# Kernel optimization log

Hardware: AMD Instinct MI355X
Metric: run time of the kernel (lower is better)

The kernel has to match this reference:

```python
import jax, jax.numpy as jnp
import numpy as np

N_NODES = 50000
N_EDGES = 400000
HID = 128
DIM_OUT = 1


def setup_inputs() -> dict:
    key = jax.random.key(0)
    ks = jax.random.split(key, 8)
    x = jax.random.normal(ks[0], (N_NODES, HID), dtype=jnp.float32)
    edge_attr = jax.random.normal(ks[1], (N_EDGES, HID), dtype=jnp.float32)
    edge_index = jax.random.randint(ks[2], (2, N_EDGES), 0, N_NODES, dtype=jnp.int64)
    # MLP params (Linear stores weight as [out,in] in torch; we use [in,out] and matmul)
    s1 = 1.0 / np.sqrt(3 * HID)
    s2 = 1.0 / np.sqrt(50)
    s3 = 1.0 / np.sqrt(25)
    W1 = jax.random.normal(ks[3], (3 * HID, 50), dtype=jnp.float32) * s1
    b1 = jnp.zeros((50,), dtype=jnp.float32)
    W2 = jax.random.normal(ks[4], (50, 25), dtype=jnp.float32) * s2
    b2 = jnp.zeros((25,), dtype=jnp.float32)
    W3 = jax.random.normal(ks[5], (25, DIM_OUT), dtype=jnp.float32) * s3
    b3 = jnp.zeros((DIM_OUT,), dtype=jnp.float32)
    return {"x": x, "edge_attr": edge_attr, "edge_index": edge_index,
            "W1": W1, "b1": b1, "W2": W2, "b2": b2, "W3": W3, "b3": b3}


def reference(x, edge_attr, edge_index, W1, b1, W2, b2, W3, b3):
    # gather endpoint features: x[edge_index.T] -> [E, 2, H] -> [E, 2H], relu
    h = jnp.take(x, edge_index.T, axis=0).reshape(-1, 2 * HID)  # [E, 2H]
    h = jax.nn.relu(h)
    h = jnp.concatenate([h, edge_attr], axis=1)  # [E, 3H]
    # 3-layer MLP (dropout = identity in eval mode)
    h = jax.nn.relu(h @ W1 + b1)
    h = jax.nn.relu(h @ W2 + b2)
    return h @ W3 + b3
```

## Files before the change

### kernel.cpp

```cpp
#include <hip/hip_runtime.h>

#define HID 128
#define PROW 104

__global__ void detect_idx_kernel(const unsigned int* __restrict__ p, int* __restrict__ flag) {
  __shared__ int s;
  if (threadIdx.x == 0) s = 0;
  __syncthreads();
  if (p[2 * threadIdx.x + 1] != 0u) atomicOr(&s, 1);
  __syncthreads();
  if (threadIdx.x == 0) *flag = s;
}

__global__ __launch_bounds__(256, 4)
void node_pre_kernel(const float* __restrict__ x, const float* __restrict__ W1,
                     float* __restrict__ P, int n_nodes) {
  __shared__ __align__(16) float a_s[32][132];
  __shared__ __align__(16) float w_s[32][64];
  const int t = threadIdx.x;
  const int half = blockIdx.y;
  const int n0 = blockIdx.x * 128;
  const int jt = t & 15, rt = t >> 4;
  float acc[8][4];
#pragma unroll
  for (int i = 0; i < 8; ++i)
#pragma unroll
    for (int q = 0; q < 4; ++q) acc[i][q] = 0.f;

  for (int kc = 0; kc < 4; ++kc) {
#pragma unroll
    for (int i = 0; i < 4; ++i) {
      int f = t + 256 * i;
      int e = f >> 3;
      int k4 = (f & 7) << 2;
      int n = n0 + e;
      float4 v = make_float4(0.f, 0.f, 0.f, 0.f);
      if (n < n_nodes) v = *(const float4*)&x[(long)n * HID + kc * 32 + k4];
      a_s[k4 + 0][e] = fmaxf(v.x, 0.f);
      a_s[k4 + 1][e] = fmaxf(v.y, 0.f);
      a_s[k4 + 2][e] = fmaxf(v.z, 0.f);
      a_s[k4 + 3][e] = fmaxf(v.w, 0.f);
    }
#pragma unroll
    for (int i = 0; i < 8; ++i) {
      int f = t + 256 * i;
      int k = f >> 6, j = f & 63;
      float w = 0.f;
      if (j < 50) w = W1[(half * 128 + kc * 32 + k) * 50 + j];
      w_s[k][j] = w;
    }
    __syncthreads();
#pragma unroll 8
    for (int kk = 0; kk < 32; ++kk) {
      float4 w4 = *(const float4*)&w_s[kk][jt * 4];
      float4 a0 = *(const float4*)&a_s[kk][rt * 8];
      float4 a1 = *(const float4*)&a_s[kk][rt * 8 + 4];
      float av[8] = {a0.x, a0.y, a0.z, a0.w, a1.x, a1.y, a1.z, a1.w};
      float wv[4] = {w4.x, w4.y, w4.z, w4.w};
#pragma unroll
      for (int ri = 0; ri < 8; ++ri)
#pragma unroll
        for (int q = 0; q < 4; ++q) acc[ri][q] = fmaf(av[ri], wv[q], acc[ri][q]);
    }
    __syncthreads();
  }
  int jb = jt * 4;
  if (jb < 50) {
#pragma unroll
    for (int ri = 0; ri < 8; ++ri) {
      int n = n0 + rt * 8 + ri;
      if (n < n_nodes) {
#pragma unroll
        for (int q = 0; q < 4; ++q) {
          int j = jb + q;
          if (j < 50) P[(long)n * PROW + half * 52 + j] = acc[ri][q];
        }
      }
    }
  }
}

__global__ __launch_bounds__(256, 4)
void edge_kernel(const float* __restrict__ ea, const void* __restrict__ eidx,
                 const float* __restrict__ W1, const float* __restrict__ b1,
                 const float* __restrict__ W2, const float* __restrict__ b2,
                 const float* __restrict__ W3, const float* __restrict__ b3,
                 const float* __restrict__ P, const int* __restrict__ flag,
                 float* __restrict__ out, int n_edges) {
  __shared__ __align__(16) union SU {
    struct { float a[32][132]; float w[32][64]; } s1;
    float h1[128][53];
  } u;
  __shared__ float w2_s[50][25];
  __shared__ float w3_s[25];
  __shared__ float b1_s[64];
  __shared__ float b2_s[25];
  __shared__ float p_s[2][128];
  __shared__ int src_s[128], dst_s[128];

  const int t = threadIdx.x;
  const int e0 = blockIdx.x * 128;

  for (int f = t; f < 1250; f += 256) ((float*)w2_s)[f] = W2[f];
  if (t < 25) { w3_s[t] = W3[t]; b2_s[t] = b2[t]; }
  if (t < 64) b1_s[t] = (t < 50) ? b1[t] : 0.f;
  const int use32 = *flag;
  if (t < 128) {
    int e = e0 + t;
    int v = 0;
    if (e < n_edges) v = use32 ? ((const int*)eidx)[e] : (int)((const long long*)eidx)[e];
    src_s[t] = v;
  } else {
    int e = e0 + (t - 128);
    int v = 0;
    if (e < n_edges)
      v = use32 ? ((const int*)eidx)[(long)n_edges + e] : (int)((const long long*)eidx)[(long)n_edges + e];
    dst_s[t - 128] = v;
  }

  const int jt = t & 15, rt = t >> 4;
  float acc[8][4];
#pragma unroll
  for (int i = 0; i < 8; ++i)
#pragma unroll
    for (int q = 0; q < 4; ++q) acc[i][q] = 0.f;

  for (int kc = 0; kc < 4; ++kc) {
#pragma unroll
    for (int i = 0; i < 4; ++i) {
      int f = t + 256 * i;
      int e = f >> 3;
      int k4 = (f & 7) << 2;
      int ee = e0 + e;
      float4 v = make_float4(0.f, 0.f, 0.f, 0.f);
      if (ee < n_edges) v = *(const float4*)&ea[(long)ee * HID + kc * 32 + k4];
      u.s1.a[k4 + 0][e] = v.x;
      u.s1.a[k4 + 1][e] = v.y;
      u.s1.a[k4 + 2][e] = v.z;
      u.s1.a[k4 + 3][e] = v.w;
    }
#pragma unroll
    for (int i = 0; i < 8; ++i) {
      int f = t + 256 * i;
      int k = f >> 6, j = f & 63;
      float w = 0.f;
      if (j < 50) w = W1[(256 + kc * 32 + k) * 50 + j];
      u.s1.w[k][j] = w;
    }
    __syncthreads();
#pragma unroll 8
    for (int kk = 0; kk < 32; ++kk) {
      float4 w4 = *(const float4*)&u.s1.w[kk][jt * 4];
      float4 a0 = *(const float4*)&u.s1.a[kk][rt * 8];
      float4 a1 = *(const float4*)&u.s1.a[kk][rt * 8 + 4];
      float av[8] = {a0.x, a0.y, a0.z, a0.w, a1.x, a1.y, a1.z, a1.w};
      float wv[4] = {w4.x, w4.y, w4.z, w4.w};
#pragma unroll
      for (int ri = 0; ri < 8; ++ri)
#pragma unroll
        for (int q = 0; q < 4; ++q) acc[ri][q] = fmaf(av[ri], wv[q], acc[ri][q]);
    }
    __syncthreads();
  }

  int jb = jt * 4;
  if (jb < 50) {
#pragma unroll
    for (int ri = 0; ri < 8; ++ri) {
      int e = rt * 8 + ri;
      int s = src_s[e], d = dst_s[e];
      float4 pa = *(const float4*)&P[(long)s * PROW + jb];
      float4 pb = *(const float4*)&P[(long)d * PROW + 52 + jb];
      float par[4] = {pa.x, pa.y, pa.z, pa.w};
      float pbr[4] = {pb.x, pb.y, pb.z, pb.w};
#pragma unroll
      for (int q = 0; q < 4; ++q) {
        int j = jb + q;
        if (j < 50) {
          float v = acc[ri][q] + par[q] + pbr[q] + b1_s[j];
          u.h1[e][j] = fmaxf(v, 0.f);
        }
      }
    }
  }
  __syncthreads();

  const int e2 = t & 127, hh = t >> 7;
  const int jb2 = hh * 13;
  float acc2[13];
#pragma unroll
  for (int jj = 0; jj < 13; ++jj) {
    int j2 = jb2 + jj;
    acc2[jj] = (j2 < 25) ? b2_s[j2] : 0.f;
  }
  for (int k2 = 0; k2 < 50; ++k2) {
    float v = u.h1[e2][k2];
#pragma unroll
    for (int jj = 0; jj < 13; ++jj) {
      int j2 = jb2 + jj;
      if (j2 < 25) acc2[jj] = fmaf(v, w2_s[k2][j2], acc2[jj]);
    }
  }
  float part = 0.f;
#pragma unroll
  for (int jj = 0; jj < 13; ++jj) {
    int j2 = jb2 + jj;
    if (j2 < 25) part += fmaxf(acc2[jj], 0.f) * w3_s[j2];
  }
  p_s[hh][e2] = part;
  __syncthreads();
  if (t < 128 && (e0 + t) < n_edges) out[e0 + t] = p_s[0][t] + p_s[1][t] + b3[0];
}

__global__ __launch_bounds__(256, 2)
void edge_naive_kernel(const float* __restrict__ x, const float* __restrict__ ea,
                       const void* __restrict__ eidx,
                       const float* __restrict__ W1, const float* __restrict__ b1,
                       const float* __restrict__ W2, const float* __restrict__ b2,
                       const float* __restrict__ W3, const float* __restrict__ b3,
                       const int* __restrict__ flag, int use32_const,
                       float* __restrict__ out, int n_edges) {
  int e = blockIdx.x * blockDim.x + threadIdx.x;
  if (e >= n_edges) return;
  int use32 = flag ? *flag : use32_const;
  long s, d;
  if (use32) {
    s = ((const int*)eidx)[e];
    d = ((const int*)eidx)[(long)n_edges + e];
  } else {
    s = (long)((const long long*)eidx)[e];
    d = (long)((const long long*)eidx)[(long)n_edges + e];
  }
  float h1[50];
#pragma unroll
  for (int j = 0; j < 50; ++j) h1[j] = b1[j];
  for (int k = 0; k < 128; ++k) {
    float v = fmaxf(x[s * HID + k], 0.f);
#pragma unroll
    for (int j = 0; j < 50; ++j) h1[j] = fmaf(v, W1[k * 50 + j], h1[j]);
  }
  for (int k = 0; k < 128; ++k) {
    float v = fmaxf(x[d * HID + k], 0.f);
#pragma unroll
    for (int j = 0; j < 50; ++j) h1[j] = fmaf(v, W1[(128 + k) * 50 + j], h1[j]);
  }
  for (int k = 0; k < 128; ++k) {
    float v = ea[(long)e * HID + k];
#pragma unroll
    for (int j = 0; j < 50; ++j) h1[j] = fmaf(v, W1[(256 + k) * 50 + j], h1[j]);
  }
  float o = b3[0];
  for (int j2 = 0; j2 < 25; ++j2) {
    float h2 = b2[j2];
#pragma unroll 10
    for (int k = 0; k < 50; ++k) h2 = fmaf(fmaxf(h1[k], 0.f), W2[k * 25 + j2], h2);
    o = fmaf(fmaxf(h2, 0.f), W3[j2], o);
  }
  out[e] = o;
}

extern "C" void kernel_launch(void* const* d_in, const int* in_sizes, int n_in,
                              void* d_out, int out_size, void* d_ws, size_t ws_size,
                              hipStream_t stream) {
  const float* x  = (const float*)d_in[0];
  const float* ea = (const float*)d_in[1];
  const void*  ei = d_in[2];
  const float* W1 = (const float*)d_in[3];
  const float* b1 = (const float*)d_in[4];
  const float* W2 = (const float*)d_in[5];
  const float* b2 = (const float*)d_in[6];
  const float* W3 = (const float*)d_in[7];
  const float* b3 = (const float*)d_in[8];
  float* out = (float*)d_out;
  const int n_nodes = in_sizes[0] / HID;
  const int n_edges = in_sizes[1] / HID;
  const size_t pbytes = (size_t)n_nodes * PROW * sizeof(float);

  if (ws_size >= pbytes + sizeof(int)) {
    float* P = (float*)d_ws;
    int* flag = (int*)((char*)d_ws + pbytes);
    hipLaunchKernelGGL(detect_idx_kernel, dim3(1), dim3(256), 0, stream,
                       (const unsigned int*)ei, flag);
    dim3 gp((n_nodes + 127) / 128, 2);
    hipLaunchKernelGGL(node_pre_kernel, gp, dim3(256), 0, stream, x, W1, P, n_nodes);
    dim3 ge((n_edges + 127) / 128);
    hipLaunchKernelGGL(edge_kernel, ge, dim3(256), 0, stream,
                       ea, ei, W1, b1, W2, b2, W3, b3, P, flag, out, n_edges);
  } else if (ws_size >= sizeof(int)) {
    int* flag = (int*)d_ws;
    hipLaunchKernelGGL(detect_idx_kernel, dim3(1), dim3(256), 0, stream,
                       (const unsigned int*)ei, flag);
    hipLaunchKernelGGL(edge_naive_kernel, dim3((n_edges + 255) / 256), dim3(256), 0, stream,
                       x, ea, ei, W1, b1, W2, b2, W3, b3, flag, 1, out, n_edges);
  } else {
    hipLaunchKernelGGL(edge_naive_kernel, dim3((n_edges + 255) / 256), dim3(256), 0, stream,
                       x, ea, ei, W1, b1, W2, b2, W3, b3, (const int*)nullptr, 1, out, n_edges);
  }
}
```

Measured before the change: 249.4 us.

## Double-buffer edge_attr tiles, preload full W1 slice, prefetch P gathers early

Restructures the edge kernel's first-layer GEMM. The whole 128x50 W1 edge slice is loaded into shared memory once instead of per chunk, and edge_attr chunks of 16 are double-buffered with register prefetch two chunks ahead, which halves the barriers per chunk. The random P gathers for the source and destination nodes are issued before the GEMM loop so their latency overlaps compute. In exchange, register pressure rises from holding 16 prefetched P float4s, and launch bounds drop to 3 blocks per SM.

```diff
diff --git a/kernel.cpp b/kernel.cpp
--- a/kernel.cpp
+++ b/kernel.cpp
@@ -2,6 +2,8 @@
 
 #define HID 128
 #define PROW 104
+#define KC 16
+#define NKC 8
 
 __global__ void detect_idx_kernel(const unsigned int* __restrict__ p, int* __restrict__ flag) {
   __shared__ int s;
@@ -80,17 +82,18 @@
   }
 }
 
-__global__ __launch_bounds__(256, 4)
+__global__ __launch_bounds__(256, 3)
 void edge_kernel(const float* __restrict__ ea, const void* __restrict__ eidx,
                  const float* __restrict__ W1, const float* __restrict__ b1,
                  const float* __restrict__ W2, const float* __restrict__ b2,
                  const float* __restrict__ W3, const float* __restrict__ b3,
                  const float* __restrict__ P, const int* __restrict__ flag,
                  float* __restrict__ out, int n_edges) {
-  __shared__ __align__(16) union SU {
-    struct { float a[32][132]; float w[32][64]; } s1;
+  __shared__ __align__(16) union WU {
+    float w[128][56];
     float h1[128][53];
   } u;
+  __shared__ __align__(16) float a_s[2][KC][132];
   __shared__ float w2_s[50][25];
   __shared__ float w3_s[25];
   __shared__ float b1_s[64];
@@ -100,6 +103,8 @@
 
   const int t = threadIdx.x;
   const int e0 = blockIdx.x * 128;
+  const int jt = t & 15, rt = t >> 4;
+  const int wj = (jt <= 12) ? jt * 4 : 48;
 
   for (int f = t; f < 1250; f += 256) ((float*)w2_s)[f] = W2[f];
   if (t < 25) { w3_s[t] = W3[t]; b2_s[t] = b2[t]; }
@@ -117,62 +122,92 @@
       v = use32 ? ((const int*)eidx)[(long)n_edges + e] : (int)((const long long*)eidx)[(long)n_edges + e];
     dst_s[t - 128] = v;
   }
-
-  const int jt = t & 15, rt = t >> 4;
+  for (int f = t; f < 128 * 64; f += 256) {
+    int r = f >> 6, j = f & 63;
+    if (j < 56) u.w[r][j] = (j < 50) ? W1[(256 + r) * 50 + j] : 0.f;
+  }
+  const int le = t >> 2;
+  const int k4 = (t & 3) << 2;
+  float4 av[2], apf[2];
+#pragma unroll
+  for (int i = 0; i < 2; ++i) {
+    int ee = e0 + le + 64 * i;
+    av[i] = make_float4(0.f, 0.f, 0.f, 0.f);
+    if (ee < n_edges) av[i] = *(const float4*)&ea[(long)ee * HID + k4];
+  }
+#pragma unroll
+  for (int i = 0; i < 2; ++i) {
+    int e = le + 64 * i;
+    a_s[0][k4 + 0][e] = av[i].x;
+    a_s[0][k4 + 1][e] = av[i].y;
+    a_s[0][k4 + 2][e] = av[i].z;
+    a_s[0][k4 + 3][e] = av[i].w;
+  }
+#pragma unroll
+  for (int i = 0; i < 2; ++i) {
+    int ee = e0 + le + 64 * i;
+    apf[i] = make_float4(0.f, 0.f, 0.f, 0.f);
+    if (ee < n_edges) apf[i] = *(const float4*)&ea[(long)ee * HID + KC + k4];
+  }
+  __syncthreads();
+
+  float4 ppa[8], ppb[8];
+  const int jb = jt * 4;
+#pragma unroll
+  for (int ri = 0; ri < 8; ++ri) {
+    int e = rt * 8 + ri;
+    long s = src_s[e], d = dst_s[e];
+    ppa[ri] = *(const float4*)&P[s * PROW + jb];
+    ppb[ri] = *(const float4*)&P[d * PROW + 52 + jb];
+  }
+
   float acc[8][4];
 #pragma unroll
   for (int i = 0; i < 8; ++i)
 #pragma unroll
     for (int q = 0; q < 4; ++q) acc[i][q] = 0.f;
 
-  for (int kc = 0; kc < 4; ++kc) {
-#pragma unroll
-    for (int i = 0; i < 4; ++i) {
-      int f = t + 256 * i;
-      int e = f >> 3;
-      int k4 = (f & 7) << 2;
-      int ee = e0 + e;
-      float4 v = make_float4(0.f, 0.f, 0.f, 0.f);
-      if (ee < n_edges) v = *(const float4*)&ea[(long)ee * HID + kc * 32 + k4];
-      u.s1.a[k4 + 0][e] = v.x;
-      u.s1.a[k4 + 1][e] = v.y;
-      u.s1.a[k4 + 2][e] = v.z;
-      u.s1.a[k4 + 3][e] = v.w;
-    }
-#pragma unroll
-    for (int i = 0; i < 8; ++i) {
-      int f = t + 256 * i;
-      int k = f >> 6, j = f & 63;
-      float w = 0.f;
-      if (j < 50) w = W1[(256 + kc * 32 + k) * 50 + j];
-      u.s1.w[k][j] = w;
+  for (int kc = 0; kc < NKC; ++kc) {
+    const int cur = kc & 1;
+#pragma unroll
+    for (int kk = 0; kk < KC; ++kk) {
+      float4 w4 = *(const float4*)&u.w[kc * KC + kk][wj];
+      float4 a0 = *(const float4*)&a_s[cur][kk][rt * 8];
+      float4 a1 = *(const float4*)&a_s[cur][kk][rt * 8 + 4];
+      float avv[8] = {a0.x, a0.y, a0.z, a0.w, a1.x, a1.y, a1.z, a1.w};
+      float wv[4] = {w4.x, w4.y, w4.z, w4.w};
+#pragma unroll
+      for (int ri = 0; ri < 8; ++ri)
+#pragma unroll
+        for (int q = 0; q < 4; ++q) acc[ri][q] = fmaf(avv[ri], wv[q], acc[ri][q]);
+    }
+    if (kc < NKC - 1) {
+#pragma unroll
+      for (int i = 0; i < 2; ++i) {
+        int e = le + 64 * i;
+        a_s[cur ^ 1][k4 + 0][e] = apf[i].x;
+        a_s[cur ^ 1][k4 + 1][e] = apf[i].y;
+        a_s[cur ^ 1][k4 + 2][e] = apf[i].z;
+        a_s[cur ^ 1][k4 + 3][e] = apf[i].w;
+      }
+    }
+    if (kc < NKC - 2) {
+#pragma unroll
+      for (int i = 0; i < 2; ++i) {
+        int ee = e0 + le + 64 * i;
+        apf[i] = make_float4(0.f, 0.f, 0.f, 0.f);
+        if (ee < n_edges) apf[i] = *(const float4*)&ea[(long)ee * HID + (kc + 2) * KC + k4];
+      }
     }
     __syncthreads();
-#pragma unroll 8
-    for (int kk = 0; kk < 32; ++kk) {
-      float4 w4 = *(const float4*)&u.s1.w[kk][jt * 4];
-      float4 a0 = *(const float4*)&u.s1.a[kk][rt * 8];
-      float4 a1 = *(const float4*)&u.s1.a[kk][rt * 8 + 4];
-      float av[8] = {a0.x, a0.y, a0.z, a0.w, a1.x, a1.y, a1.z, a1.w};
-      float wv[4] = {w4.x, w4.y, w4.z, w4.w};
-#pragma unroll
-      for (int ri = 0; ri < 8; ++ri)
-#pragma unroll
-        for (int q = 0; q < 4; ++q) acc[ri][q] = fmaf(av[ri], wv[q], acc[ri][q]);
-    }
-    __syncthreads();
-  }
-
-  int jb = jt * 4;
+  }
+
   if (jb < 50) {
 #pragma unroll
     for (int ri = 0; ri < 8; ++ri) {
       int e = rt * 8 + ri;
-      int s = src_s[e], d = dst_s[e];
-      float4 pa = *(const float4*)&P[(long)s * PROW + jb];
-      float4 pb = *(const float4*)&P[(long)d * PROW + 52 + jb];
-      float par[4] = {pa.x, pa.y, pa.z, pa.w};
-      float pbr[4] = {pb.x, pb.y, pb.z, pb.w};
+      float par[4] = {ppa[ri].x, ppa[ri].y, ppa[ri].z, ppa[ri].w};
+      float pbr[4] = {ppb[ri].x, ppb[ri].y, ppb[ri].z, ppb[ri].w};
 #pragma unroll
       for (int q = 0; q < 4; ++q) {
         int j = jb + q;
```

Result: slower. 930.2 us (+273.0%).

## Double-buffer edge_attr tiles via direct global-to-LDS loads in edge kernel

Applied to the files above, without the earlier changes.

The edge kernel now streams edge_attr in 16-wide K chunks into a double-buffered row-major LDS tile using global_load_lds, so the load for chunk k+2 overlaps compute on chunk k. The whole 128x50 edge slice of W1 is preloaded into LDS once instead of reloading per chunk, and the edge-to-thread mapping becomes interleaved (rt + 16*ri). Launch bounds drop from 4 to 2 blocks per CU to allow more registers. The aim is to hide global-load latency and cut barriers and redundant weight loads, at the cost of more LDS per block and lower occupancy. It relies on async LDS loads being complete at each barrier.

```diff
diff --git a/kernel.cpp b/kernel.cpp
--- a/kernel.cpp
+++ b/kernel.cpp
@@ -2,6 +2,13 @@
 
 #define HID 128
 #define PROW 104
+#define KC 16
+#define NKC 8
+
+__device__ __forceinline__ void gload16(const void* g, void* l) {
+  __builtin_amdgcn_global_load_lds((const __attribute__((address_space(1))) void*)g,
+                                   (__attribute__((address_space(3))) void*)l, 16, 0, 0);
+}
 
 __global__ void detect_idx_kernel(const unsigned int* __restrict__ p, int* __restrict__ flag) {
   __shared__ int s;
@@ -80,17 +87,18 @@
   }
 }
 
-__global__ __launch_bounds__(256, 4)
+__global__ __launch_bounds__(256, 2)
 void edge_kernel(const float* __restrict__ ea, const void* __restrict__ eidx,
                  const float* __restrict__ W1, const float* __restrict__ b1,
                  const float* __restrict__ W2, const float* __restrict__ b2,
                  const float* __restrict__ W3, const float* __restrict__ b3,
                  const float* __restrict__ P, const int* __restrict__ flag,
                  float* __restrict__ out, int n_edges) {
-  __shared__ __align__(16) union SU {
-    struct { float a[32][132]; float w[32][64]; } s1;
-    float h1[128][53];
+  __shared__ __align__(16) union WU {
+    float w[128][52];
+    float h1[128][51];
   } u;
+  __shared__ __align__(16) float a_s[2][128][KC];
   __shared__ float w2_s[50][25];
   __shared__ float w3_s[25];
   __shared__ float b1_s[64];
@@ -100,6 +108,29 @@
 
   const int t = threadIdx.x;
   const int e0 = blockIdx.x * 128;
+  const int jt = t & 15, rt = t >> 4;
+  const int wj = (jt <= 12) ? jt * 4 : 48;
+  const int wv = t >> 6;
+  const int ln = t & 63;
+  const bool full = (e0 + 128 <= n_edges);
+
+  auto stage = [&](int buf, int kc) {
+    if (full) {
+#pragma unroll
+      for (int c = 0; c < 2; ++c) {
+        int et = wv * 32 + c * 16 + (ln >> 2);
+        gload16(&ea[(long)(e0 + et) * HID + kc * KC + (ln & 3) * 4],
+                &a_s[buf][et][(ln & 3) * 4]);
+      }
+    } else {
+      for (int f = t; f < 512; f += 256) {
+        int et = f >> 2, q = f & 3;
+        float4 v = make_float4(0.f, 0.f, 0.f, 0.f);
+        if (e0 + et < n_edges) v = *(const float4*)&ea[(long)(e0 + et) * HID + kc * KC + q * 4];
+        *(float4*)&a_s[buf][et][q * 4] = v;
+      }
+    }
+  };
 
   for (int f = t; f < 1250; f += 256) ((float*)w2_s)[f] = W2[f];
   if (t < 25) { w3_s[t] = W3[t]; b2_s[t] = b2[t]; }
@@ -117,60 +148,53 @@
       v = use32 ? ((const int*)eidx)[(long)n_edges + e] : (int)((const long long*)eidx)[(long)n_edges + e];
     dst_s[t - 128] = v;
   }
-
-  const int jt = t & 15, rt = t >> 4;
+  for (int f = t; f < 128 * 52; f += 256) {
+    int r = f / 52, j = f % 52;
+    u.w[r][j] = (j < 50) ? W1[(256 + r) * 50 + j] : 0.f;
+  }
+  stage(0, 0);
+  stage(1, 1);
+  __syncthreads();
+
   float acc[8][4];
 #pragma unroll
   for (int i = 0; i < 8; ++i)
 #pragma unroll
     for (int q = 0; q < 4; ++q) acc[i][q] = 0.f;
 
-  for (int kc = 0; kc < 4; ++kc) {
-#pragma unroll
-    for (int i = 0; i < 4; ++i) {
-      int f = t + 256 * i;
-      int e = f >> 3;
-      int k4 = (f & 7) << 2;
-      int ee = e0 + e;
-      float4 v = make_float4(0.f, 0.f, 0.f, 0.f);
-      if (ee < n_edges) v = *(const float4*)&ea[(long)ee * HID + kc * 32 + k4];
-      u.s1.a[k4 + 0][e] = v.x;
-      u.s1.a[k4 + 1][e] = v.y;
-      u.s1.a[k4 + 2][e] = v.z;
-      u.s1.a[k4 + 3][e] = v.w;
-    }
-#pragma unroll
-    for (int i = 0; i < 8; ++i) {
-      int f = t + 256 * i;
-      int k = f >> 6, j = f & 63;
-      float w = 0.f;
-      if (j < 50) w = W1[(256 + kc * 32 + k) * 50 + j];
-      u.s1.w[k][j] = w;
+  for (int kc = 0; kc < NKC; ++kc) {
+    const int cur = kc & 1;
+#pragma unroll
+    for (int kq = 0; kq < KC / 4; ++kq) {
+      float4 w4[4];
+#pragma unroll
+      for (int i = 0; i < 4; ++i)
+        w4[i] = *(const float4*)&u.w[kc * KC + kq * 4 + i][wj];
+#pragma unroll
+      for (int ri = 0; ri < 8; ++ri) {
+        float4 a4 = *(const float4*)&a_s[cur][rt + 16 * ri][kq * 4];
+        float am[4] = {a4.x, a4.y, a4.z, a4.w};
+#pragma unroll
+        for (int kk = 0; kk < 4; ++kk) {
+          acc[ri][0] = fmaf(am[kk], w4[kk].x, acc[ri][0]);
+          acc[ri][1] = fmaf(am[kk], w4[kk].y, acc[ri][1]);
+          acc[ri][2] = fmaf(am[kk], w4[kk].z, acc[ri][2]);
+          acc[ri][3] = fmaf(am[kk], w4[kk].w, acc[ri][3]);
+        }
+      }
     }
     __syncthreads();
-#pragma unroll 8
-    for (int kk = 0; kk < 32; ++kk) {
-      float4 w4 = *(const float4*)&u.s1.w[kk][jt * 4];
-      float4 a0 = *(const float4*)&u.s1.a[kk][rt * 8];
-      float4 a1 = *(const float4*)&u.s1.a[kk][rt * 8 + 4];
-      float av[8] = {a0.x, a0.y, a0.z, a0.w, a1.x, a1.y, a1.z, a1.w};
-      float wv[4] = {w4.x, w4.y, w4.z, w4.w};
-#pragma unroll
-      for (int ri = 0; ri < 8; ++ri)
-#pragma unroll
-        for (int q = 0; q < 4; ++q) acc[ri][q] = fmaf(av[ri], wv[q], acc[ri][q]);
-    }
-    __syncthreads();
-  }
-
-  int jb = jt * 4;
+    if (kc + 2 < NKC) stage(cur, kc + 2);
+  }
+
+  const int jb = jt * 4;
   if (jb < 50) {
 #pragma unroll
     for (int ri = 0; ri < 8; ++ri) {
-      int e = rt * 8 + ri;
-      int s = src_s[e], d = dst_s[e];
-      float4 pa = *(const float4*)&P[(long)s * PROW + jb];
-      float4 pb = *(const float4*)&P[(long)d * PROW + 52 + jb];
+      int e = rt + 16 * ri;
+      long s = src_s[e], d = dst_s[e];
+      float4 pa = *(const float4*)&P[s * PROW + jb];
+      float4 pb = *(const float4*)&P[d * PROW + 52 + jb];
       float par[4] = {pa.x, pa.y, pa.z, pa.w};
       float pbr[4] = {pb.x, pb.y, pb.z, pb.w};
 #pragma unroll
```

Measured after the change: 355.1 us. +42.4%, slower.

## Preload full W1 edge slice to LDS and register-prefetch edge_attr chunks

Applied to the files above, without the earlier changes.

The edge kernel now loads the whole 128x50 edge_attr block of W1 into shared memory once instead of per 32-wide k chunk. It processes edge_attr in 16-wide chunks and prefetches the next chunk into registers while computing the current one, which hides global load latency behind the FMAs. W2, W3 and b2 are now read straight from global memory (wave-uniform, so likely scalar or cached loads) rather than staged in LDS. In exchange there are twice as many k-chunk barriers and a larger up-front W1 staging cost per block.

```diff
diff --git a/kernel.cpp b/kernel.cpp
--- a/kernel.cpp
+++ b/kernel.cpp
@@ -2,6 +2,8 @@
 
 #define HID 128
 #define PROW 104
+#define KC 16
+#define NKC 8
 
 __global__ void detect_idx_kernel(const unsigned int* __restrict__ p, int* __restrict__ flag) {
   __shared__ int s;
@@ -88,21 +90,21 @@
                  const float* __restrict__ P, const int* __restrict__ flag,
                  float* __restrict__ out, int n_edges) {
   __shared__ __align__(16) union SU {
-    struct { float a[32][132]; float w[32][64]; } s1;
+    struct {
+      float w[128][52];
+      float a[KC][132];
+    } gs;
     float h1[128][53];
   } u;
-  __shared__ float w2_s[50][25];
-  __shared__ float w3_s[25];
   __shared__ float b1_s[64];
-  __shared__ float b2_s[25];
   __shared__ float p_s[2][128];
   __shared__ int src_s[128], dst_s[128];
 
   const int t = threadIdx.x;
   const int e0 = blockIdx.x * 128;
-
-  for (int f = t; f < 1250; f += 256) ((float*)w2_s)[f] = W2[f];
-  if (t < 25) { w3_s[t] = W3[t]; b2_s[t] = b2[t]; }
+  const int jt = t & 15, rt = t >> 4;
+  const int wj = (jt <= 12) ? jt * 4 : 48;
+
   if (t < 64) b1_s[t] = (t < 50) ? b1[t] : 0.f;
   const int use32 = *flag;
   if (t < 128) {
@@ -117,60 +119,71 @@
       v = use32 ? ((const int*)eidx)[(long)n_edges + e] : (int)((const long long*)eidx)[(long)n_edges + e];
     dst_s[t - 128] = v;
   }
-
-  const int jt = t & 15, rt = t >> 4;
+  for (int f = t; f < 128 * 52; f += 256) {
+    int r = f / 52, j = f % 52;
+    u.gs.w[r][j] = (j < 50) ? W1[(256 + r) * 50 + j] : 0.f;
+  }
+  const int ae = t >> 1;
+  const int ak = (t & 1) << 3;
+  float4 av0, av1;
+  {
+    float4 z = make_float4(0.f, 0.f, 0.f, 0.f);
+    av0 = z; av1 = z;
+    if (e0 + ae < n_edges) {
+      av0 = *(const float4*)&ea[(long)(e0 + ae) * HID + ak];
+      av1 = *(const float4*)&ea[(long)(e0 + ae) * HID + ak + 4];
+    }
+  }
+
   float acc[8][4];
 #pragma unroll
   for (int i = 0; i < 8; ++i)
 #pragma unroll
     for (int q = 0; q < 4; ++q) acc[i][q] = 0.f;
 
-  for (int kc = 0; kc < 4; ++kc) {
-#pragma unroll
-    for (int i = 0; i < 4; ++i) {
-      int f = t + 256 * i;
-      int e = f >> 3;
-      int k4 = (f & 7) << 2;
-      int ee = e0 + e;
-      float4 v = make_float4(0.f, 0.f, 0.f, 0.f);
-      if (ee < n_edges) v = *(const float4*)&ea[(long)ee * HID + kc * 32 + k4];
-      u.s1.a[k4 + 0][e] = v.x;
-      u.s1.a[k4 + 1][e] = v.y;
-      u.s1.a[k4 + 2][e] = v.z;
-      u.s1.a[k4 + 3][e] = v.w;
-    }
-#pragma unroll
-    for (int i = 0; i < 8; ++i) {
-      int f = t + 256 * i;
-      int k = f >> 6, j = f & 63;
-      float w = 0.f;
-      if (j < 50) w = W1[(256 + kc * 32 + k) * 50 + j];
-      u.s1.w[k][j] = w;
-    }
+#pragma unroll 1
+  for (int kc = 0; kc < NKC; ++kc) {
+    u.gs.a[ak + 0][ae] = av0.x;
+    u.gs.a[ak + 1][ae] = av0.y;
+    u.gs.a[ak + 2][ae] = av0.z;
+    u.gs.a[ak + 3][ae] = av0.w;
+    u.gs.a[ak + 4][ae] = av1.x;
+    u.gs.a[ak + 5][ae] = av1.y;
+    u.gs.a[ak + 6][ae] = av1.z;
+    u.gs.a[ak + 7][ae] = av1.w;
     __syncthreads();
-#pragma unroll 8
-    for (int kk = 0; kk < 32; ++kk) {
-      float4 w4 = *(const float4*)&u.s1.w[kk][jt * 4];
-      float4 a0 = *(const float4*)&u.s1.a[kk][rt * 8];
-      float4 a1 = *(const float4*)&u.s1.a[kk][rt * 8 + 4];
-      float av[8] = {a0.x, a0.y, a0.z, a0.w, a1.x, a1.y, a1.z, a1.w};
+    if (kc + 1 < NKC) {
+      float4 z = make_float4(0.f, 0.f, 0.f, 0.f);
+      float4 n0 = z, n1 = z;
+      if (e0 + ae < n_edges) {
+        n0 = *(const float4*)&ea[(long)(e0 + ae) * HID + (kc + 1) * KC + ak];
+        n1 = *(const float4*)&ea[(long)(e0 + ae) * HID + (kc + 1) * KC + ak + 4];
+      }
+      av0 = n0; av1 = n1;
+    }
+#pragma unroll
+    for (int kk = 0; kk < KC; ++kk) {
+      float4 w4 = *(const float4*)&u.gs.w[kc * KC + kk][wj];
+      float4 a0 = *(const float4*)&u.gs.a[kk][rt * 8];
+      float4 a1 = *(const float4*)&u.gs.a[kk][rt * 8 + 4];
+      float am[8] = {a0.x, a0.y, a0.z, a0.w, a1.x, a1.y, a1.z, a1.w};
       float wv[4] = {w4.x, w4.y, w4.z, w4.w};
 #pragma unroll
       for (int ri = 0; ri < 8; ++ri)
 #pragma unroll
-        for (int q = 0; q < 4; ++q) acc[ri][q] = fmaf(av[ri], wv[q], acc[ri][q]);
+        for (int q = 0; q < 4; ++q) acc[ri][q] = fmaf(am[ri], wv[q], acc[ri][q]);
     }
     __syncthreads();
   }
 
-  int jb = jt * 4;
+  const int jb = jt * 4;
   if (jb < 50) {
 #pragma unroll
     for (int ri = 0; ri < 8; ++ri) {
       int e = rt * 8 + ri;
-      int s = src_s[e], d = dst_s[e];
-      float4 pa = *(const float4*)&P[(long)s * PROW + jb];
-      float4 pb = *(const float4*)&P[(long)d * PROW + 52 + jb];
+      long s = src_s[e], d = dst_s[e];
+      float4 pa = *(const float4*)&P[s * PROW + jb];
+      float4 pb = *(const float4*)&P[d * PROW + 52 + jb];
       float par[4] = {pa.x, pa.y, pa.z, pa.w};
       float pbr[4] = {pb.x, pb.y, pb.z, pb.w};
 #pragma unroll
@@ -191,21 +204,21 @@
 #pragma unroll
   for (int jj = 0; jj < 13; ++jj) {
     int j2 = jb2 + jj;
-    acc2[jj] = (j2 < 25) ? b2_s[j2] : 0.f;
+    acc2[jj] = (j2 < 25) ? b2[j2] : 0.f;
   }
   for (int k2 = 0; k2 < 50; ++k2) {
     float v = u.h1[e2][k2];
 #pragma unroll
     for (int jj = 0; jj < 13; ++jj) {
       int j2 = jb2 + jj;
-      if (j2 < 25) acc2[jj] = fmaf(v, w2_s[k2][j2], acc2[jj]);
+      if (j2 < 25) acc2[jj] = fmaf(v, W2[k2 * 25 + j2], acc2[jj]);
     }
   }
   float part = 0.f;
 #pragma unroll
   for (int jj = 0; jj < 13; ++jj) {
     int j2 = jb2 + jj;
-    if (j2 < 25) part += fmaxf(acc2[jj], 0.f) * w3_s[j2];
+    if (j2 < 25) part += fmaxf(acc2[jj], 0.f) * W3[j2];
   }
   p_s[hh][e2] = part;
   __syncthreads();
@@ -277,7 +290,7 @@
   const size_t pbytes = (size_t)n_nodes * PROW * sizeof(float);
 
   if (ws_size >= pbytes + sizeof(int)) {
-    float* P = (float*)d_ws;
+    float* P  = (float*)d_ws;
     int* flag = (int*)((char*)d_ws + pbytes);
     hipLaunchKernelGGL(detect_idx_kernel, dim3(1), dim3(256), 0, stream,
                        (const unsigned int*)ei, flag);
```

Result: slower. 419.1 us (+68.0%).
